# Performance work log

Hardware: AMD Instinct MI355X
Metric: run time of the kernel (lower is better)

Reference implementation:

```python
import math
import jax, jax.numpy as jnp
import numpy as np

GROUPS = 8
EPS = 1e-5
NUM_HEADS = 8

def setup_inputs() -> dict:
    key = jax.random.key(0)
    ks = jax.random.split(key, 4)
    B, C, H, W = 4, 256, 48, 48
    x = jax.random.normal(ks[0], (B, C, H, W), dtype=jnp.float32)
    qkv_weight = jax.random.normal(ks[1], (3 * C, C), dtype=jnp.float32) * (1.0 / math.sqrt(C))
    qkv_bias = jnp.zeros((3 * C,), dtype=jnp.float32)
    proj_weight = jax.random.normal(ks[2], (C, C), dtype=jnp.float32) * (1.0 / math.sqrt(C))
    proj_bias = jnp.zeros((C,), dtype=jnp.float32)
    gn_weight = jnp.ones((C,), dtype=jnp.float32)
    gn_bias = jnp.zeros((C,), dtype=jnp.float32)
    return {"x": x, "gn_weight": gn_weight, "gn_bias": gn_bias,
            "qkv_weight": qkv_weight, "qkv_bias": qkv_bias,
            "proj_weight": proj_weight, "proj_bias": proj_bias}

def group_norm(x, weight, bias):
    B, C, H, W = x.shape
    xg = x.reshape(B, GROUPS, -1)  # [B, G, (C/G)*H*W]
    mean = jnp.mean(xg, axis=-1, keepdims=True)
    var = jnp.mean(jnp.square(xg - mean), axis=-1, keepdims=True)
    xn = ((xg - mean) * jax.lax.rsqrt(var + EPS)).reshape(B, C, H, W)
    return xn * weight[None, :, None, None] + bias[None, :, None, None]

def reference(x, gn_weight, gn_bias, qkv_weight, qkv_bias, proj_weight, proj_bias):
    B, C, H, W = x.shape
    T = H * W
    h = NUM_HEADS
    hd = C // h
    n = group_norm(x, gn_weight, gn_bias).reshape(B, C, T)
    qkv = jnp.einsum('oc,bct->bot', qkv_weight, n) + qkv_bias[None, :, None]
    q, k, v = jnp.split(qkv, 3, axis=1)  # each [B, C, T]
    q = q.reshape(B, h, hd, T)
    k = k.reshape(B, h, hd, T)
    v = v.reshape(B, h, hd, T)
    scale = 1.0 / math.sqrt(hd)
    scores = jnp.einsum('bhdt,bhds->bhts', q, k) * scale  # [B, h, T, T]
    attn = jax.nn.softmax(scores, axis=-1)
    out = jnp.einsum('bhts,bhds->bhdt', attn, v).reshape(B, C, T)
    out = jnp.einsum('oc,bct->bot', proj_weight, out) + proj_bias[None, :, None]
    return x + out.reshape(B, C, H, W)
```

## Files before the change

kernel.cpp:

```cpp
#include <hip/hip_runtime.h>

#define B_ 4
#define C_ 256
#define T_ 2304
#define HD 32
#define GSZ (32 * T_)
#define SCL2E (0.17677669529663687f * 1.44269504088896f)

typedef short bf16x8 __attribute__((ext_vector_type(8)));
typedef float f32x4 __attribute__((ext_vector_type(4)));
typedef unsigned int u32x2 __attribute__((ext_vector_type(2)));

__device__ inline unsigned short f2bf(float f) {
  unsigned int u = __float_as_uint(f);
  return (unsigned short)((u + 0x7FFFu + ((u >> 16) & 1u)) >> 16);
}

__device__ inline float fexp2(float x) {
  float r;
  asm("v_exp_f32 %0, %1" : "=v"(r) : "v"(x));
  return r;
}

__device__ inline unsigned cvtpk(float lo, float hi) {
  unsigned r;
  asm("v_cvt_pk_bf16_f32 %0, %1, %2" : "=v"(r) : "v"(lo), "v"(hi));
  return r;
}

__global__ void prep(const float* wq, const float* wp, const float* x,
                     unsigned short* oq, unsigned short* op, float* ws1) {
  if (blockIdx.x < 1024) {
    int i = blockIdx.x * 256 + threadIdx.x;
    const int n1 = 3 * C_ * C_;
    if (i < n1) oq[i] = f2bf(wq[i]);
    else        op[i - n1] = f2bf(wp[i - n1]);
    return;
  }
  int bid = blockIdx.x - 1024;
  int bg = bid >> 3, sl = bid & 7;
  const float4* p = (const float4*)(x + (size_t)bg * GSZ + sl * (GSZ / 8));
  float s = 0.f, q = 0.f;
  for (int it = 0; it < 9; ++it) {
    float4 v = p[it * 256 + threadIdx.x];
    s += v.x + v.y + v.z + v.w;
    q += v.x * v.x + v.y * v.y + v.z * v.z + v.w * v.w;
  }
  for (int off = 32; off; off >>= 1) {
    s += __shfl_down(s, off);
    q += __shfl_down(q, off);
  }
  __shared__ float red[8];
  int w = threadIdx.x >> 6;
  if ((threadIdx.x & 63) == 0) { red[w * 2] = s; red[w * 2 + 1] = q; }
  __syncthreads();
  if (threadIdx.x == 0) {
    float S = red[0] + red[2] + red[4] + red[6];
    float Q = red[1] + red[3] + red[5] + red[7];
    ws1[bid * 2] = S;
    ws1[bid * 2 + 1] = Q;
  }
}

__global__ void gn_norm(const float* x, const float* ws1, const float* gamma,
                        const float* beta, unsigned short* nT) {
  int b = blockIdx.y, t0 = blockIdx.x * 32;
  __shared__ unsigned short tile[32 * 264];
  __shared__ float stl[16];
  int tid = threadIdx.x;
  if (tid < 8) {
    float S = 0.f, Q = 0.f;
    for (int sl = 0; sl < 8; ++sl) {
      S += ws1[((b * 8 + tid) * 8 + sl) * 2];
      Q += ws1[((b * 8 + tid) * 8 + sl) * 2 + 1];
    }
    float mean = S / (float)GSZ;
    float var = Q / (float)GSZ - mean * mean;
    stl[tid * 2] = mean;
    stl[tid * 2 + 1] = rsqrtf(var + 1e-5f);
  }
  __syncthreads();
#pragma unroll
  for (int it = 0; it < 8; ++it) {
    int qd = it * 256 + tid;
    int c = qd >> 3, tq = qd & 7;
    float4 v = *(const float4*)&x[((size_t)b * C_ + c) * T_ + t0 + tq * 4];
    int g = c >> 5;
    float mean = stl[g * 2], rstd = stl[g * 2 + 1];
    float sc = rstd * gamma[c];
    float sh = beta[c] - mean * sc;
    tile[(tq * 4 + 0) * 264 + c] = f2bf(v.x * sc + sh);
    tile[(tq * 4 + 1) * 264 + c] = f2bf(v.y * sc + sh);
    tile[(tq * 4 + 2) * 264 + c] = f2bf(v.z * sc + sh);
    tile[(tq * 4 + 3) * 264 + c] = f2bf(v.w * sc + sh);
  }
  __syncthreads();
#pragma unroll
  for (int it = 0; it < 4; ++it) {
    int qd = it * 256 + tid;
    int tt = qd >> 5, c8 = (qd & 31) * 8;
    *(uint4*)&nT[((size_t)b * T_ + t0 + tt) * C_ + c8] = *(const uint4*)&tile[tt * 264 + c8];
  }
}

__global__ __launch_bounds__(256) void qkv_gemm(const unsigned short* W, const unsigned short* nT,
                                                const float* bias, unsigned short* qT,
                                                unsigned short* kT, unsigned short* vW) {
  __shared__ short As[64 * 264];
  __shared__ short Bs[64 * 264];
  int b = blockIdx.z;
  int tid = threadIdx.x;
  int lane = tid & 63, w = tid >> 6;
  int r16 = lane & 15, g4 = lane >> 4;
  int y = blockIdx.y;
  int type = y >> 2;

  {
    int r = tid >> 2, c8 = (tid & 3) * 8;
    const unsigned short* Ag = W + (size_t)(y * 64 + r) * C_ + c8;
    const unsigned short* Bg = nT + (size_t)b * T_ * C_ + (size_t)(blockIdx.x * 64 + r) * C_ + c8;
    short* Ad = &As[r * 264 + c8];
    short* Bd = &Bs[r * 264 + c8];
#pragma unroll
    for (int p = 0; p < 8; ++p) {
      *(int4*)(Ad + p * 32) = *(const int4*)(Ag + p * 32);
      *(int4*)(Bd + p * 32) = *(const int4*)(Bg + p * 32);
    }
  }
  __syncthreads();

  int mw = (w >> 1) * 32, nw = (w & 1) * 32;
  f32x4 acc[2][2] = {};
#pragma unroll
  for (int ks = 0; ks < 8; ++ks) {
    bf16x8 a0 = *(const bf16x8*)&As[(mw + r16) * 264 + ks * 32 + g4 * 8];
    bf16x8 a1 = *(const bf16x8*)&As[(mw + 16 + r16) * 264 + ks * 32 + g4 * 8];
    bf16x8 b0 = *(const bf16x8*)&Bs[(nw + r16) * 264 + ks * 32 + g4 * 8];
    bf16x8 b1 = *(const bf16x8*)&Bs[(nw + 16 + r16) * 264 + ks * 32 + g4 * 8];
    acc[0][0] = __builtin_amdgcn_mfma_f32_16x16x32_bf16(a0, b0, acc[0][0], 0, 0, 0);
    acc[0][1] = __builtin_amdgcn_mfma_f32_16x16x32_bf16(a0, b1, acc[0][1], 0, 0, 0);
    acc[1][0] = __builtin_amdgcn_mfma_f32_16x16x32_bf16(a1, b0, acc[1][0], 0, 0, 0);
    acc[1][1] = __builtin_amdgcn_mfma_f32_16x16x32_bf16(a1, b1, acc[1][1], 0, 0, 0);
  }
  __syncthreads();

  short* tt = As;
#pragma unroll
  for (int mi = 0; mi < 2; ++mi) {
#pragma unroll
    for (int ni = 0; ni < 2; ++ni) {
      int t_loc = (w & 1) * 32 + ni * 16 + r16;
      int o_loc = (w >> 1) * 32 + mi * 16 + g4 * 4;
      int o = y * 64 + o_loc;
      float v0 = acc[mi][ni][0] + bias[o + 0];
      float v1 = acc[mi][ni][1] + bias[o + 1];
      float v2 = acc[mi][ni][2] + bias[o + 2];
      float v3 = acc[mi][ni][3] + bias[o + 3];
      if (type == 0) { v0 *= SCL2E; v1 *= SCL2E; v2 *= SCL2E; v3 *= SCL2E; }
      if (type < 2) {
        u32x2 pw = {cvtpk(v0, v1), cvtpk(v2, v3)};
        *(u32x2*)&tt[t_loc * 72 + o_loc] = pw;
      } else {
        tt[(o_loc + 0) * 72 + t_loc] = f2bf(v0);
        tt[(o_loc + 1) * 72 + t_loc] = f2bf(v1);
        tt[(o_loc + 2) * 72 + t_loc] = f2bf(v2);
        tt[(o_loc + 3) * 72 + t_loc] = f2bf(v3);
      }
    }
  }
  __syncthreads();
  if (type < 2) {
    unsigned short* dst = (type == 0) ? qT : kT;
    int obase = y * 64 - type * 256;
    int t_loc = tid >> 2;
    int tg = blockIdx.x * 64 + t_loc;
#pragma unroll
    for (int half = 0; half < 2; ++half) {
      int o_loc = half * 32 + (tid & 3) * 8;
      int o2 = obase + o_loc;
      int hh = o2 >> 5, d = o2 & 31;
      *(uint4*)&dst[(((size_t)b * 8 + hh) * T_ + tg) * HD + d] = *(const uint4*)&tt[t_loc * 72 + o_loc];
    }
  } else {
    int obase = y * 64 - 512;
    int o_loc = tid >> 2;
    int o2 = obase + o_loc;
    int hh = o2 >> 5, d = o2 & 31;
    unsigned short* vdst = vW + ((size_t)(b * 8 + hh) * HD + d) * T_ + blockIdx.x * 64;
#pragma unroll
    for (int half = 0; half < 2; ++half) {
      int t_loc = half * 32 + (tid & 3) * 8;
      *(uint4*)&vdst[t_loc] = *(const uint4*)&tt[o_loc * 72 + t_loc];
    }
  }
}

__global__ __launch_bounds__(256) void attn(const unsigned short* qT, const unsigned short* kT,
                                            const unsigned short* vW, unsigned short* aT) {
  int b = blockIdx.z, h = blockIdx.y, qt = blockIdx.x;
  int tid = threadIdx.x, lane = tid & 63, w = tid >> 6;
  int part = w >> 1, wsub = w & 1;
  int r16 = lane & 15, g4 = lane >> 4;
  __shared__ short Ks[2][2][64 * 40];
  __shared__ short Vs[2][2][32 * 72];
  const unsigned short* qB = qT + ((size_t)b * 8 + h) * T_ * HD;
  const unsigned short* kB = kT + ((size_t)b * 8 + h) * T_ * HD;
  const unsigned short* vB = vW + ((size_t)b * 8 + h) * HD * T_;
  int qbase = qt * 64 + wsub * 32;
  bf16x8 qfA = *(const bf16x8*)(qB + (qbase + r16) * HD + g4 * 8);
  bf16x8 qfB = *(const bf16x8*)(qB + (qbase + 16 + r16) * HD + g4 * 8);
  const short OB = (short)0x3F80;
  const bf16x8 ones = {OB, OB, OB, OB, OB, OB, OB, OB};
  f32x4 accA0 = {}, accA1 = {}, accB0 = {}, accB1 = {};
  f32x4 accLA = {}, accLB = {};
  int t0 = part * 18;

  int tp = tid & 127;
  int krow = tp >> 2, kcol = (tid & 3) * 8;
  int vrow = tp >> 3, vcol = (tid & 7) * 8;
  const unsigned short* kSrc = kB + (size_t)krow * HD + kcol;
  const unsigned short* vSrc = vB + (size_t)vrow * T_ + vcol;
  int4 rgK0, rgK1, rgV0, rgV1;

  union PU { unsigned u[4]; bf16x8 v; };
  union VU { int2 d2[2]; bf16x8 v; };

#define LOADT(t_) {                                                               \
    const unsigned short* k_ = kSrc + (t_) * 64 * HD;                             \
    rgK0 = *(const int4*)k_;                                                      \
    rgK1 = *(const int4*)(k_ + 32 * HD);                                          \
    const unsigned short* v_ = vSrc + (t_) * 64;                                  \
    rgV0 = *(const int4*)v_;                                                      \
    rgV1 = *(const int4*)(v_ + (size_t)16 * T_);                                  \
  }

#define STORET(bi) {                                                              \
    short* kD = &Ks[part][bi][krow * 40 + kcol];                                  \
    *(int4*)kD = rgK0;                                                            \
    *(int4*)(kD + 32 * 40) = rgK1;                                                \
    short* vD = &Vs[part][bi][vrow * 72 + vcol];                                  \
    *(int4*)vD = rgV0;                                                            \
    *(int4*)(vD + 16 * 72) = rgV1;                                                \
  }

#define SUBTILE(qf, accL, acc0, acc1) {                                           \
    f32x4 z = {};                                                                 \
    f32x4 s0 = __builtin_amdgcn_mfma_f32_16x16x32_bf16(kf0, qf, z, 0, 0, 0);      \
    f32x4 s1 = __builtin_amdgcn_mfma_f32_16x16x32_bf16(kf1, qf, z, 0, 0, 0);      \
    f32x4 s2 = __builtin_amdgcn_mfma_f32_16x16x32_bf16(kf2, qf, z, 0, 0, 0);      \
    f32x4 s3 = __builtin_amdgcn_mfma_f32_16x16x32_bf16(kf3, qf, z, 0, 0, 0);      \
    float p0 = fexp2(s0[0]), p1 = fexp2(s0[1]), p2 = fexp2(s0[2]), p3 = fexp2(s0[3]); \
    float p4 = fexp2(s1[0]), p5 = fexp2(s1[1]), p6 = fexp2(s1[2]), p7 = fexp2(s1[3]); \
    float p8 = fexp2(s2[0]), p9 = fexp2(s2[1]), pa = fexp2(s2[2]), pb = fexp2(s2[3]); \
    float pc = fexp2(s3[0]), pd = fexp2(s3[1]), pe = fexp2(s3[2]), pf = fexp2(s3[3]); \
    PU w0, w1;                                                                    \
    w0.u[0] = cvtpk(p0, p1); w0.u[1] = cvtpk(p2, p3);                             \
    w0.u[2] = cvtpk(p4, p5); w0.u[3] = cvtpk(p6, p7);                             \
    w1.u[0] = cvtpk(p8, p9); w1.u[1] = cvtpk(pa, pb);                             \
    w1.u[2] = cvtpk(pc, pd); w1.u[3] = cvtpk(pe, pf);                             \
    accL = __builtin_amdgcn_mfma_f32_16x16x32_bf16(ones, w0.v, accL, 0, 0, 0);    \
    accL = __builtin_amdgcn_mfma_f32_16x16x32_bf16(ones, w1.v, accL, 0, 0, 0);    \
    acc0 = __builtin_amdgcn_mfma_f32_16x16x32_bf16(vf00.v, w0.v, acc0, 0, 0, 0);  \
    acc1 = __builtin_amdgcn_mfma_f32_16x16x32_bf16(vf01.v, w0.v, acc1, 0, 0, 0);  \
    acc0 = __builtin_amdgcn_mfma_f32_16x16x32_bf16(vf10.v, w1.v, acc0, 0, 0, 0);  \
    acc1 = __builtin_amdgcn_mfma_f32_16x16x32_bf16(vf11.v, w1.v, acc1, 0, 0, 0);  \
  }

  LOADT(t0)
  STORET(0)
  LOADT(t0 + 1)
  __syncthreads();

  for (int t = 0; t < 18; ++t) {
    int bi = t & 1;
    if (t < 17) STORET(bi ^ 1)
    if (t < 16) LOADT(t0 + t + 2)

    const short* Kc = &Ks[part][bi][0];
    const short* Vc = &Vs[part][bi][0];
    bf16x8 kf0 = *(const bf16x8*)&Kc[(r16) * 40 + g4 * 8];
    bf16x8 kf1 = *(const bf16x8*)&Kc[(16 + r16) * 40 + g4 * 8];
    bf16x8 kf2 = *(const bf16x8*)&Kc[(32 + r16) * 40 + g4 * 8];
    bf16x8 kf3 = *(const bf16x8*)&Kc[(48 + r16) * 40 + g4 * 8];
    VU vf00, vf01, vf10, vf11;
    {
      const short* vr0 = Vc + r16 * 72;
      const short* vr1 = Vc + (16 + r16) * 72;
      vf00.d2[0] = *(const int2*)(vr0 + 4 * g4);
      vf00.d2[1] = *(const int2*)(vr0 + 16 + 4 * g4);
      vf01.d2[0] = *(const int2*)(vr1 + 4 * g4);
      vf01.d2[1] = *(const int2*)(vr1 + 16 + 4 * g4);
      vf10.d2[0] = *(const int2*)(vr0 + 32 + 4 * g4);
      vf10.d2[1] = *(const int2*)(vr0 + 48 + 4 * g4);
      vf11.d2[0] = *(const int2*)(vr1 + 32 + 4 * g4);
      vf11.d2[1] = *(const int2*)(vr1 + 48 + 4 * g4);
    }

    SUBTILE(qfA, accLA, accA0, accA1)
    SUBTILE(qfB, accLB, accB0, accB1)

    __syncthreads();
  }

  float lA = accLA[0];
  float lB = accLB[0];

  float* ex = (float*)&Ks[1][0][0];
  float* lex = ex + 2048;
  if (part == 1) {
    f32x4* dst = (f32x4*)&ex[(wsub * 64 + lane) * 16];
    dst[0] = accA0; dst[1] = accA1; dst[2] = accB0; dst[3] = accB1;
    lex[(wsub * 64 + lane) * 2] = lA;
    lex[(wsub * 64 + lane) * 2 + 1] = lB;
  }
  __syncthreads();
  if (part == 0) {
    const f32x4* src = (const f32x4*)&ex[(wsub * 64 + lane) * 16];
    accA0 += src[0]; accA1 += src[1]; accB0 += src[2]; accB1 += src[3];
    lA += lex[(wsub * 64 + lane) * 2];
    lB += lex[(wsub * 64 + lane) * 2 + 1];
    float invA = 1.f / lA;
    float invB = 1.f / lB;
    unsigned short* oA = aT + ((size_t)b * T_ + qbase + r16) * C_ + h * HD + 4 * g4;
    unsigned short* oB = aT + ((size_t)b * T_ + qbase + 16 + r16) * C_ + h * HD + 4 * g4;
    u32x2 wA0 = {cvtpk(accA0[0] * invA, accA0[1] * invA), cvtpk(accA0[2] * invA, accA0[3] * invA)};
    u32x2 wA1 = {cvtpk(accA1[0] * invA, accA1[1] * invA), cvtpk(accA1[2] * invA, accA1[3] * invA)};
    u32x2 wB0 = {cvtpk(accB0[0] * invB, accB0[1] * invB), cvtpk(accB0[2] * invB, accB0[3] * invB)};
    u32x2 wB1 = {cvtpk(accB1[0] * invB, accB1[1] * invB), cvtpk(accB1[2] * invB, accB1[3] * invB)};
    *(u32x2*)oA = wA0;
    *(u32x2*)(oA + 16) = wA1;
    *(u32x2*)oB = wB0;
    *(u32x2*)(oB + 16) = wB1;
  }
#undef LOADT
#undef STORET
#undef SUBTILE
}

__global__ __launch_bounds__(256) void proj_gemm(const unsigned short* W, const unsigned short* aT,
                                                 const float* bias, const float* x, float* out) {
  __shared__ short As[64 * 264];
  __shared__ short Bs[64 * 264];
  int b = blockIdx.z;
  int tid = threadIdx.x;
  int lane = tid & 63, w = tid >> 6;
  int r16 = lane & 15, g4 = lane >> 4;

  {
    int r = tid >> 2, c8 = (tid & 3) * 8;
    const unsigned short* Ag = W + (size_t)(blockIdx.y * 64 + r) * C_ + c8;
    const unsigned short* Bg = aT + (size_t)b * T_ * C_ + (size_t)(blockIdx.x * 64 + r) * C_ + c8;
    short* Ad = &As[r * 264 + c8];
    short* Bd = &Bs[r * 264 + c8];
#pragma unroll
    for (int p = 0; p < 8; ++p) {
      *(int4*)(Ad + p * 32) = *(const int4*)(Ag + p * 32);
      *(int4*)(Bd + p * 32) = *(const int4*)(Bg + p * 32);
    }
  }
  __syncthreads();

  int mw = (w >> 1) * 32, nw = (w & 1) * 32;
  f32x4 acc[2][2] = {};
#pragma unroll
  for (int ks = 0; ks < 8; ++ks) {
    bf16x8 a0 = *(const bf16x8*)&As[(mw + r16) * 264 + ks * 32 + g4 * 8];
    bf16x8 a1 = *(const bf16x8*)&As[(mw + 16 + r16) * 264 + ks * 32 + g4 * 8];
    bf16x8 b0 = *(const bf16x8*)&Bs[(nw + r16) * 264 + ks * 32 + g4 * 8];
    bf16x8 b1 = *(const bf16x8*)&Bs[(nw + 16 + r16) * 264 + ks * 32 + g4 * 8];
    acc[0][0] = __builtin_amdgcn_mfma_f32_16x16x32_bf16(a0, b0, acc[0][0], 0, 0, 0);
    acc[0][1] = __builtin_amdgcn_mfma_f32_16x16x32_bf16(a0, b1, acc[0][1], 0, 0, 0);
    acc[1][0] = __builtin_amdgcn_mfma_f32_16x16x32_bf16(a1, b0, acc[1][0], 0, 0, 0);
    acc[1][1] = __builtin_amdgcn_mfma_f32_16x16x32_bf16(a1, b1, acc[1][1], 0, 0, 0);
  }
  int m0 = blockIdx.y * 64 + mw;
  int n0 = blockIdx.x * 64 + nw;
  for (int mi = 0; mi < 2; ++mi)
    for (int ni = 0; ni < 2; ++ni) {
      int t = n0 + ni * 16 + r16;
      for (int r = 0; r < 4; ++r) {
        int o = m0 + mi * 16 + g4 * 4 + r;
        size_t idx = ((size_t)b * C_ + o) * T_ + t;
        out[idx] = x[idx] + acc[mi][ni][r] + bias[o];
      }
    }
}

extern "C" void kernel_launch(void* const* d_in, const int* in_sizes, int n_in,
                              void* d_out, int out_size, void* d_ws, size_t ws_size,
                              hipStream_t stream) {
  const float* x  = (const float*)d_in[0];
  const float* gw = (const float*)d_in[1];
  const float* gb = (const float*)d_in[2];
  const float* wq = (const float*)d_in[3];
  const float* bq = (const float*)d_in[4];
  const float* wp = (const float*)d_in[5];
  const float* bp = (const float*)d_in[6];

  char* ws = (char*)d_ws;
  float* ws1 = (float*)ws;
  unsigned short* wqb = (unsigned short*)(ws + 4096);
  unsigned short* wpb = wqb + 3 * C_ * C_;
  unsigned short* nT  = wpb + C_ * C_;
  const size_t NE = (size_t)B_ * T_ * C_;
  unsigned short* qT = nT + NE;
  unsigned short* kT = qT + NE;
  unsigned short* vW = kT + NE;
  unsigned short* aT = vW + NE;

  prep<<<1280, 256, 0, stream>>>(wq, wp, x, wqb, wpb, ws1);
  gn_norm<<<dim3(72, 4), 256, 0, stream>>>(x, ws1, gw, gb, nT);
  qkv_gemm<<<dim3(36, 12, 4), 256, 0, stream>>>(wqb, nT, bq, qT, kT, vW);
  attn<<<dim3(36, 8, 4), 256, 0, stream>>>(qT, kT, vW, aT);
  proj_gemm<<<dim3(36, 4, 4), 256, 0, stream>>>(wpb, aT, bp, x, (float*)d_out);
}
```

Before: 79.86 us.

## Permute V tile layout for 16-byte LDS loads and batch QK MFMAs

The QKV GEMM epilogue now writes V with a permuted token order, so each lane's eight P·V operand values sit together. The attention loop can then fetch each V fragment with one 16-byte LDS read instead of two 8-byte reads. All eight score MFMAs for both query subtiles are also issued before the softmax/PV stages, and the PV and row-sum MFMAs are interleaved, giving the scheduler more independent work to hide latency. The cost is extra live score registers and index arithmetic in the V store.

After: 81.32 us. No clear change (+1.8%).

```diff
diff --git a/kernel.cpp b/kernel.cpp
--- a/kernel.cpp
+++ b/kernel.cpp
@@ -161,10 +161,13 @@
         u32x2 pw = {cvtpk(v0, v1), cvtpk(v2, v3)};
         *(u32x2*)&tt[t_loc * 72 + o_loc] = pw;
       } else {
-        tt[(o_loc + 0) * 72 + t_loc] = f2bf(v0);
-        tt[(o_loc + 1) * 72 + t_loc] = f2bf(v1);
-        tt[(o_loc + 2) * 72 + t_loc] = f2bf(v2);
-        tt[(o_loc + 3) * 72 + t_loc] = f2bf(v3);
+        int s5 = t_loc & 31;
+        int e = s5 >> 4, r4 = s5 & 15;
+        int tp = (t_loc & 32) | (((r4 >> 2) << 3) + (e << 2) + (r4 & 3));
+        tt[(o_loc + 0) * 72 + tp] = f2bf(v0);
+        tt[(o_loc + 1) * 72 + tp] = f2bf(v1);
+        tt[(o_loc + 2) * 72 + tp] = f2bf(v2);
+        tt[(o_loc + 3) * 72 + tp] = f2bf(v3);
       }
     }
   }
@@ -223,7 +226,6 @@
   int4 rgK0, rgK1, rgV0, rgV1;
 
   union PU { unsigned u[4]; bf16x8 v; };
-  union VU { int2 d2[2]; bf16x8 v; };
 
 #define LOADT(t_) {                                                               \
     const unsigned short* k_ = kSrc + (t_) * 64 * HD;                             \
@@ -243,12 +245,7 @@
     *(int4*)(vD + 16 * 72) = rgV1;                                                \
   }
 
-#define SUBTILE(qf, accL, acc0, acc1) {                                           \
-    f32x4 z = {};                                                                 \
-    f32x4 s0 = __builtin_amdgcn_mfma_f32_16x16x32_bf16(kf0, qf, z, 0, 0, 0);      \
-    f32x4 s1 = __builtin_amdgcn_mfma_f32_16x16x32_bf16(kf1, qf, z, 0, 0, 0);      \
-    f32x4 s2 = __builtin_amdgcn_mfma_f32_16x16x32_bf16(kf2, qf, z, 0, 0, 0);      \
-    f32x4 s3 = __builtin_amdgcn_mfma_f32_16x16x32_bf16(kf3, qf, z, 0, 0, 0);      \
+#define SMPV(s0, s1, s2, s3, accL, acc0, acc1) {                                  \
     float p0 = fexp2(s0[0]), p1 = fexp2(s0[1]), p2 = fexp2(s0[2]), p3 = fexp2(s0[3]); \
     float p4 = fexp2(s1[0]), p5 = fexp2(s1[1]), p6 = fexp2(s1[2]), p7 = fexp2(s1[3]); \
     float p8 = fexp2(s2[0]), p9 = fexp2(s2[1]), pa = fexp2(s2[2]), pb = fexp2(s2[3]); \
@@ -258,12 +255,12 @@
     w0.u[2] = cvtpk(p4, p5); w0.u[3] = cvtpk(p6, p7);                             \
     w1.u[0] = cvtpk(p8, p9); w1.u[1] = cvtpk(pa, pb);                             \
     w1.u[2] = cvtpk(pc, pd); w1.u[3] = cvtpk(pe, pf);                             \
+    acc0 = __builtin_amdgcn_mfma_f32_16x16x32_bf16(vf00, w0.v, acc0, 0, 0, 0);    \
+    acc1 = __builtin_amdgcn_mfma_f32_16x16x32_bf16(vf01, w0.v, acc1, 0, 0, 0);    \
     accL = __builtin_amdgcn_mfma_f32_16x16x32_bf16(ones, w0.v, accL, 0, 0, 0);    \
+    acc0 = __builtin_amdgcn_mfma_f32_16x16x32_bf16(vf10, w1.v, acc0, 0, 0, 0);    \
+    acc1 = __builtin_amdgcn_mfma_f32_16x16x32_bf16(vf11, w1.v, acc1, 0, 0, 0);    \
     accL = __builtin_amdgcn_mfma_f32_16x16x32_bf16(ones, w1.v, accL, 0, 0, 0);    \
-    acc0 = __builtin_amdgcn_mfma_f32_16x16x32_bf16(vf00.v, w0.v, acc0, 0, 0, 0);  \
-    acc1 = __builtin_amdgcn_mfma_f32_16x16x32_bf16(vf01.v, w0.v, acc1, 0, 0, 0);  \
-    acc0 = __builtin_amdgcn_mfma_f32_16x16x32_bf16(vf10.v, w1.v, acc0, 0, 0, 0);  \
-    acc1 = __builtin_amdgcn_mfma_f32_16x16x32_bf16(vf11.v, w1.v, acc1, 0, 0, 0);  \
   }
 
   LOADT(t0)
@@ -282,22 +279,23 @@
     bf16x8 kf1 = *(const bf16x8*)&Kc[(16 + r16) * 40 + g4 * 8];
     bf16x8 kf2 = *(const bf16x8*)&Kc[(32 + r16) * 40 + g4 * 8];
     bf16x8 kf3 = *(const bf16x8*)&Kc[(48 + r16) * 40 + g4 * 8];
-    VU vf00, vf01, vf10, vf11;
-    {
-      const short* vr0 = Vc + r16 * 72;
-      const short* vr1 = Vc + (16 + r16) * 72;
-      vf00.d2[0] = *(const int2*)(vr0 + 4 * g4);
-      vf00.d2[1] = *(const int2*)(vr0 + 16 + 4 * g4);
-      vf01.d2[0] = *(const int2*)(vr1 + 4 * g4);
-      vf01.d2[1] = *(const int2*)(vr1 + 16 + 4 * g4);
-      vf10.d2[0] = *(const int2*)(vr0 + 32 + 4 * g4);
-      vf10.d2[1] = *(const int2*)(vr0 + 48 + 4 * g4);
-      vf11.d2[0] = *(const int2*)(vr1 + 32 + 4 * g4);
-      vf11.d2[1] = *(const int2*)(vr1 + 48 + 4 * g4);
-    }
-
-    SUBTILE(qfA, accLA, accA0, accA1)
-    SUBTILE(qfB, accLB, accB0, accB1)
+    bf16x8 vf00 = *(const bf16x8*)&Vc[r16 * 72 + 8 * g4];
+    bf16x8 vf01 = *(const bf16x8*)&Vc[(16 + r16) * 72 + 8 * g4];
+    bf16x8 vf10 = *(const bf16x8*)&Vc[r16 * 72 + 32 + 8 * g4];
+    bf16x8 vf11 = *(const bf16x8*)&Vc[(16 + r16) * 72 + 32 + 8 * g4];
+
+    f32x4 z = {};
+    f32x4 sA0 = __builtin_amdgcn_mfma_f32_16x16x32_bf16(kf0, qfA, z, 0, 0, 0);
+    f32x4 sA1 = __builtin_amdgcn_mfma_f32_16x16x32_bf16(kf1, qfA, z, 0, 0, 0);
+    f32x4 sA2 = __builtin_amdgcn_mfma_f32_16x16x32_bf16(kf2, qfA, z, 0, 0, 0);
+    f32x4 sA3 = __builtin_amdgcn_mfma_f32_16x16x32_bf16(kf3, qfA, z, 0, 0, 0);
+    f32x4 sB0 = __builtin_amdgcn_mfma_f32_16x16x32_bf16(kf0, qfB, z, 0, 0, 0);
+    f32x4 sB1 = __builtin_amdgcn_mfma_f32_16x16x32_bf16(kf1, qfB, z, 0, 0, 0);
+    f32x4 sB2 = __builtin_amdgcn_mfma_f32_16x16x32_bf16(kf2, qfB, z, 0, 0, 0);
+    f32x4 sB3 = __builtin_amdgcn_mfma_f32_16x16x32_bf16(kf3, qfB, z, 0, 0, 0);
+
+    SMPV(sA0, sA1, sA2, sA3, accLA, accA0, accA1)
+    SMPV(sB0, sB1, sB2, sB3, accLB, accB0, accB1)
 
     __syncthreads();
   }
@@ -334,7 +332,7 @@
   }
 #undef LOADT
 #undef STORET
-#undef SUBTILE
+#undef SMPV
 }
 
 __global__ __launch_bounds__(256) void proj_gemm(const unsigned short* W, const unsigned short* aT,
```
